# Optimization experiments

Hardware: AMD Instinct MI355X
Metric: run time of the kernel (lower is better)

The kernel has to match this reference:

```python
import jax, jax.numpy as jnp
import numpy as np

N, IN_FEAT, OUT_FEAT, H = 4096, 256, 256, 8
D = OUT_FEAT // H  # per-head dim = 32
ADJ_DENSITY = 0.05


def setup_inputs() -> dict:
    key = jax.random.key(0)
    kx, kw, kb, ka, kadj = jax.random.split(key, 5)
    x = jax.random.normal(kx, (N, IN_FEAT), dtype=jnp.float32)
    # eqx.nn.Linear params: weight [out, in], bias [out]
    W = jax.random.normal(kw, (OUT_FEAT, IN_FEAT), dtype=jnp.float32) * (1.0 / np.sqrt(IN_FEAT))
    b = jax.random.normal(kb, (OUT_FEAT,), dtype=jnp.float32) * 0.01
    a = jax.random.normal(ka, (H, 2 * D), dtype=jnp.float32)
    adj_matrix = jax.random.bernoulli(kadj, ADJ_DENSITY, (N, N)).astype(jnp.float32)
    return {"x": x, "W": W, "b": b, "a": a, "adj_matrix": adj_matrix}


def reference(x, W, b, a, adj_matrix):
    num_nodes = x.shape[0]
    num_heads = a.shape[0]
    half = a.shape[1] // 2
    # projection: [N, H*D] -> [N, H, D]
    node_feats = (x @ W.T + b).reshape(num_nodes, num_heads, half)
    # per-head additive attention halves -> [N, H]
    logit_parent = (node_feats * a[None, :, :half]).sum(axis=-1)
    logit_child = (node_feats * a[None, :, half:]).sum(axis=-1)
    # [N, N, H] dense logits via broadcast-add
    attn_logits = logit_parent[:, None, :] + logit_child[None, :, :]
    attn_logits = jax.nn.leaky_relu(attn_logits, 0.2)
    # NOTE: faithful to source — masked entries set to 0.0 (not -inf)
    attn_logits = jnp.where(jnp.abs(adj_matrix)[..., None] != 0.0, attn_logits, 0.0)
    attn_probs = jax.nn.softmax(attn_logits, axis=1)
    out = jnp.einsum('ijh,jhc->ihc', attn_probs, node_feats)
    return out.reshape(num_nodes, -1)
```

## Files before the change

### kernel.cpp

```cpp
#include <hip/hip_runtime.h>

#define NN    4096
#define OF    256
#define NH    8
#define MAXNZ 384

typedef __attribute__((ext_vector_type(8))) short short8;
typedef __attribute__((ext_vector_type(4))) float f32x4;

__device__ __forceinline__ float bf2f(unsigned int u) {
    union { unsigned int i; float f; } v; v.i = u << 16; return v.f;
}
__device__ __forceinline__ unsigned short f2bf(float f) {
    union { float f; unsigned int i; } v; v.f = f;
    unsigned int x = v.i;
    return (unsigned short)((x + 0x7fffu + ((x >> 16) & 1u)) >> 16);
}
__device__ __forceinline__ unsigned int pk2bf(float a, float b) {
    return (unsigned int)f2bf(a) | ((unsigned int)f2bf(b) << 16);
}

__global__ __launch_bounds__(256) void k_pre(
    const float* __restrict__ adjf, const float* __restrict__ Wf,
    int* __restrict__ flag, unsigned short* __restrict__ Wbh,
    unsigned short* __restrict__ Wbl, float* __restrict__ zbase)
{
    __shared__ int viol;
    int t = threadIdx.x;
    int gid = blockIdx.x * 256 + t;
    if (t == 0) viol = 0;
    __syncthreads();
    int bad = 0;
    for (int k = t; k < NN; k += 256) {
        float v = adjf[k];
        if (!(v == 0.0f || v == 1.0f)) bad = 1;
    }
    if (bad) atomicAdd(&viol, 1);
    __syncthreads();
    int f = viol > 0;
    if (t == 0) *flag = f;

    zbase[gid] = 0.f;
    if (gid < 256) zbase[65536 + gid] = 0.f;
    if (!f) {
        float v = Wf[gid];
        unsigned short h = f2bf(v);
        Wbh[gid] = h; Wbl[gid] = f2bf(v - bf2f(h));
    }
}

__global__ __launch_bounds__(256) void k_main(
    const void* __restrict__ xraw, const void* __restrict__ Wraw,
    const void* __restrict__ braw, const void* __restrict__ araw,
    const float* __restrict__ adjf, const int* __restrict__ flag,
    const unsigned short* __restrict__ Wbh, const unsigned short* __restrict__ Wbl,
    unsigned short* __restrict__ nfb, float* __restrict__ lp,
    float* __restrict__ lc, float* __restrict__ Stot,
    unsigned short* __restrict__ csr, int* __restrict__ nnz)
{
    __shared__ unsigned short xh[16][264], xl[16][264];
    __shared__ int wtot[4];

    int f = *flag;
    int t = threadIdx.x;
    int wave = t >> 6;
    int lane = t & 63;
    int bid = blockIdx.x;
    int bdiv3 = bid / 3;

    if (bid - bdiv3*3 == 0) {
        int tid  = bdiv3 * 4 + wave;
        int mt = tid >> 4, nt = tid & 15;
        int lr = lane & 15;
        int kq = (lane >> 4) * 8;

        if (!f) {
            const float* xsrc = (const float*)xraw + (size_t)mt * 4096;
            #pragma unroll
            for (int q = 0; q < 16; q++) {
                int e = t + 256*q;
                float v = xsrc[e];
                unsigned short h = f2bf(v);
                xh[e >> 8][e & 255] = h;
                xl[e >> 8][e & 255] = f2bf(v - bf2f(h));
            }
            __syncthreads();
        }

        size_t wo = (size_t)(nt*16 + lr)*OF + kq;
        f32x4 acc = {0.f, 0.f, 0.f, 0.f};
        if (f) {
            const short8* xp = reinterpret_cast<const short8*>(
                (const unsigned short*)xraw + (size_t)(mt*16 + lr)*OF + kq);
            const short8* wp = reinterpret_cast<const short8*>(
                (const unsigned short*)Wraw + wo);
            #pragma unroll
            for (int kk = 0; kk < OF/32; kk++)
                acc = __builtin_amdgcn_mfma_f32_16x16x32_bf16(xp[kk*4], wp[kk*4], acc, 0, 0, 0);
        } else {
            const short8* wh = reinterpret_cast<const short8*>(Wbh + wo);
            const short8* wl = reinterpret_cast<const short8*>(Wbl + wo);
            #pragma unroll
            for (int kk = 0; kk < OF/32; kk++) {
                short8 ah = *reinterpret_cast<const short8*>(&xh[lr][kk*32 + kq]);
                short8 al = *reinterpret_cast<const short8*>(&xl[lr][kk*32 + kq]);
                short8 bh = wh[kk*4], bl = wl[kk*4];
                acc = __builtin_amdgcn_mfma_f32_16x16x32_bf16(ah, bh, acc, 0, 0, 0);
                acc = __builtin_amdgcn_mfma_f32_16x16x32_bf16(ah, bl, acc, 0, 0, 0);
                acc = __builtin_amdgcn_mfma_f32_16x16x32_bf16(al, bh, acc, 0, 0, 0);
            }
        }

        int col  = nt*16 + lr;
        int row0 = mt*16 + (lane >> 4) * 4;
        int h = col >> 5, cc = col & 31;
        float bias, apar, achd;
        if (f) {
            bias = bf2f((unsigned int)((const unsigned short*)braw)[col]);
            apar = bf2f((unsigned int)((const unsigned short*)araw)[h*64 + cc]);
            achd = bf2f((unsigned int)((const unsigned short*)araw)[h*64 + 32 + cc]);
        } else {
            bias = ((const float*)braw)[col];
            apar = ((const float*)araw)[h*64 + cc];
            achd = ((const float*)araw)[h*64 + 32 + cc];
        }
        float st = 0.f, pr[4], cr[4];
        #pragma unroll
        for (int r = 0; r < 4; r++) {
            float v = acc[r] + bias;
            nfb[(size_t)(row0 + r) * OF + col] = f2bf(v);
            st += v;
            pr[r] = v * apar;
            cr[r] = v * achd;
        }
        #pragma unroll
        for (int m = 1; m <= 8; m <<= 1) {
            #pragma unroll
            for (int r = 0; r < 4; r++) {
                pr[r] += __shfl_xor(pr[r], m, 64);
                cr[r] += __shfl_xor(cr[r], m, 64);
            }
        }
        if ((lane & 15) == 0) {
            #pragma unroll
            for (int r = 0; r < 4; r++) {
                atomicAdd(&lp[(row0 + r) * NH + h], pr[r]);
                atomicAdd(&lc[(row0 + r) * NH + h], cr[r]);
            }
        }
        st += __shfl_down(st, 16, 64);
        st += __shfl_down(st, 32, 64);
        if (lane < 16) atomicAdd(&Stot[col], st);
    } else {
        int sid = bid - bdiv3 - 1;
        int r    = sid*2 + (wave >> 1);
        int half = wave & 1;

        unsigned int m32 = 0;
        if (f) {
            const uint4* ap = reinterpret_cast<const uint4*>(
                (const unsigned short*)adjf + (size_t)r * NN + half * 2048);
            #pragma unroll
            for (int g = 0; g < 4; g++) {
                uint4 v = ap[lane + 64*g];
                unsigned int wd[4] = {v.x, v.y, v.z, v.w};
                #pragma unroll
                for (int u = 0; u < 4; u++) {
                    if (wd[u] & 0xffffu) m32 |= 1u << (g*8 + 2*u);
                    if (wd[u] >> 16)     m32 |= 1u << (g*8 + 2*u + 1);
                }
            }
        } else {
            const uint4* ap = reinterpret_cast<const uint4*>(
                adjf + (size_t)r * NN + half * 2048);
            #pragma unroll
            for (int g = 0; g < 8; g++) {
                uint4 v = ap[lane + 64*g];
                if (v.x) m32 |= 1u << (g*4);
                if (v.y) m32 |= 1u << (g*4 + 1);
                if (v.z) m32 |= 1u << (g*4 + 2);
                if (v.w) m32 |= 1u << (g*4 + 3);
            }
        }

        int pc = __popc(m32);
        int pref = pc;
        #pragma unroll
        for (int off = 1; off < 64; off <<= 1) {
            int u = __shfl_up(pref, off, 64);
            if (lane >= off) pref += u;
        }
        if (lane == 63) wtot[wave] = pref;
        __syncthreads();
        int base = (wave == 1) ? wtot[0] : (wave == 3) ? wtot[2] : 0;
        if (lane == 0) {
            if (wave == 0) nnz[r] = min(wtot[0] + wtot[1], MAXNZ);
            if (wave == 2) nnz[r] = min(wtot[2] + wtot[3], MAXNZ);
        }
        int pos = base + pref - pc;
        unsigned int mm = m32;
        int jb = half * 2048;
        while (mm && pos < MAXNZ) {
            int q = __builtin_ctz(mm);
            mm &= mm - 1;
            int j = f ? (jb + lane*8 + ((q >> 3) << 9) + (q & 7))
                      : (jb + lane*4 + ((q >> 2) << 8) + (q & 3));
            csr[(size_t)r * MAXNZ + pos++] = (unsigned short)j;
        }
    }
}

__global__ __launch_bounds__(256, 8) void k_attn(
    const int* __restrict__ flag, const unsigned short* __restrict__ csr,
    const int* __restrict__ nnz,
    const float* __restrict__ lp, const float* __restrict__ lc,
    const unsigned short* __restrict__ nfb, const float* __restrict__ Stot,
    void* __restrict__ outv)
{
    __shared__ float lps[NH];
    __shared__ int   jro[MAXNZ];
    __shared__ float wlist[MAXNZ][NH];
    __shared__ float zred[256];
    __shared__ float gred[3][256];

    int i = blockIdx.x;
    int t = threadIdx.x;
    int lane = t & 63, wid = t >> 6;
    int f = *flag;
    if (t < NH) lps[t] = lp[i*NH + t];
    int n = min(nnz[i], MAXNZ);

    if (t < MAXNZ/8) {
        uint4 v = reinterpret_cast<const uint4*>(csr + (size_t)i * MAXNZ)[t];
        unsigned int ws[4] = {v.x, v.y, v.z, v.w};
        #pragma unroll
        for (int u = 0; u < 4; u++) {
            jro[t*8 + 2*u]     = (int)(ws[u] & 0xffffu) * OF;
            jro[t*8 + 2*u + 1] = (int)(ws[u] >> 16) * OF;
        }
    }
    __syncthreads();

    int h8 = t & 7, c32 = t >> 3;
    float lph = lps[h8];
    float zp = 0.f;
    int k3 = c32;
    for (; k3 + 32 < n; k3 += 64) {
        int j0 = jro[k3] >> 5, j1 = jro[k3 + 32] >> 5;
        float l0 = lc[j0 + h8], l1 = lc[j1 + h8];
        float s0 = lph + l0; s0 = s0 > 0.f ? s0 : 0.2f * s0;
        float s1 = lph + l1; s1 = s1 > 0.f ? s1 : 0.2f * s1;
        float w0 = __expf(fminf(s0, 70.f)) - 1.f;
        float w1 = __expf(fminf(s1, 70.f)) - 1.f;
        wlist[k3][h8] = w0; wlist[k3 + 32][h8] = w1;
        zp += w0 + w1;
    }
    if (k3 < n) {
        float s = lph + lc[(jro[k3] >> 5) + h8];
        s = s > 0.f ? s : 0.2f * s;
        float w = __expf(fminf(s, 70.f)) - 1.f;
        wlist[k3][h8] = w;
        zp += w;
    }
    zred[t] = zp;
    __syncthreads();

    int hh = lane >> 3;
    int c4 = lane * 4;
    float a0 = 0.f, a1 = 0.f, a2 = 0.f, a3 = 0.f;
    int k = wid;
    for (; k + 28 < n; k += 32) {
        int jj[8]; float ww[8];
        #pragma unroll
        for (int u = 0; u < 8; u++) {
            jj[u] = __builtin_amdgcn_readfirstlane(jro[k + 4*u]);
            ww[u] = wlist[k + 4*u][hh];
        }
        uint2 d[8];
        #pragma unroll
        for (int u = 0; u < 8; u++)
            d[u] = *reinterpret_cast<const uint2*>(nfb + jj[u] + c4);
        #pragma unroll
        for (int u = 0; u < 8; u++) {
            a0 += ww[u] * bf2f(d[u].x & 0xffffu);
            a1 += ww[u] * bf2f(d[u].x >> 16);
            a2 += ww[u] * bf2f(d[u].y & 0xffffu);
            a3 += ww[u] * bf2f(d[u].y >> 16);
        }
    }
    for (; k < n; k += 4) {
        int j = __builtin_amdgcn_readfirstlane(jro[k]);
        float w = wlist[k][hh];
        uint2 d = *reinterpret_cast<const uint2*>(nfb + j + c4);
        a0 += w * bf2f(d.x & 0xffffu);
        a1 += w * bf2f(d.x >> 16);
        a2 += w * bf2f(d.y & 0xffffu);
        a3 += w * bf2f(d.y >> 16);
    }
    if (wid) {
        gred[wid-1][c4]   = a0; gred[wid-1][c4+1] = a1;
        gred[wid-1][c4+2] = a2; gred[wid-1][c4+3] = a3;
    }
    __syncthreads();

    if (wid == 0) {
        float z = zred[lane] + zred[lane+64] + zred[lane+128] + zred[lane+192];
        z += __shfl_down(z, 32, 64);
        z += __shfl_down(z, 16, 64);
        z += __shfl_down(z, 8, 64);
        float zfull = __shfl(z, hh, 64);
        float iz = 1.0f / (4096.0f + zfull);
        a0 += gred[0][c4]   + gred[1][c4]   + gred[2][c4];
        a1 += gred[0][c4+1] + gred[1][c4+1] + gred[2][c4+1];
        a2 += gred[0][c4+2] + gred[1][c4+2] + gred[2][c4+2];
        a3 += gred[0][c4+3] + gred[1][c4+3] + gred[2][c4+3];
        float4 stv = *reinterpret_cast<const float4*>(Stot + c4);
        float o0 = (stv.x + a0) * iz;
        float o1 = (stv.y + a1) * iz;
        float o2 = (stv.z + a2) * iz;
        float o3 = (stv.w + a3) * iz;
        if (f) {
            uint2 pk; pk.x = pk2bf(o0, o1); pk.y = pk2bf(o2, o3);
            *reinterpret_cast<uint2*>((unsigned short*)outv + (size_t)i*OF + c4) = pk;
        } else {
            float4 o = {o0, o1, o2, o3};
            *reinterpret_cast<float4*>((float*)outv + (size_t)i*OF + c4) = o;
        }
    }
}

extern "C" void kernel_launch(void* const* d_in, const int* in_sizes, int n_in,
                              void* d_out, int out_size, void* d_ws, size_t ws_size,
                              hipStream_t stream) {
    const void* x   = d_in[0];
    const void* W   = d_in[1];
    const void* b   = d_in[2];
    const void* a   = d_in[3];
    const void* adj = d_in[4];

    char* ws = (char*)d_ws;
    const size_t MB = 1024u*1024u, KB = 1024u;
    unsigned short* nfb  = (unsigned short*)(ws);
    float*          lp   = (float*)(ws + 2*MB);
    float*          lc   = (float*)(ws + 2*MB + 128*KB);
    float*          Stot = (float*)(ws + 2*MB + 256*KB);
    int*            flag = (int*)(ws + 2*MB + 257*KB);
    unsigned short* csr  = (unsigned short*)(ws + 2*MB + 258*KB);
    int*            nnz  = (int*)(ws + 5*MB + 258*KB);
    unsigned short* Wbh  = (unsigned short*)(ws + 6*MB);
    unsigned short* Wbl  = (unsigned short*)(ws + 6*MB + 128*KB);

    k_pre  <<<256,  256, 0, stream>>>((const float*)adj, (const float*)W,
                                      flag, Wbh, Wbl, lp);
    k_main <<<3072, 256, 0, stream>>>(x, W, b, a, (const float*)adj, flag,
                                      Wbh, Wbl, nfb, lp, lc, Stot, csr, nnz);
    k_attn <<<NN,   256, 0, stream>>>(flag, csr, nnz, lp, lc, nfb, Stot, d_out);
}
```

Before: 155.0 us.

## Fold preprocessing kernel into main kernel and split W to bf16 hi/lo inline

```diff
diff --git a/kernel.cpp b/kernel.cpp
--- a/kernel.cpp
+++ b/kernel.cpp
@@ -20,53 +20,35 @@
     return (unsigned int)f2bf(a) | ((unsigned int)f2bf(b) << 16);
 }
 
-__global__ __launch_bounds__(256) void k_pre(
-    const float* __restrict__ adjf, const float* __restrict__ Wf,
-    int* __restrict__ flag, unsigned short* __restrict__ Wbh,
-    unsigned short* __restrict__ Wbl, float* __restrict__ zbase)
-{
-    __shared__ int viol;
-    int t = threadIdx.x;
-    int gid = blockIdx.x * 256 + t;
-    if (t == 0) viol = 0;
-    __syncthreads();
-    int bad = 0;
-    for (int k = t; k < NN; k += 256) {
-        float v = adjf[k];
-        if (!(v == 0.0f || v == 1.0f)) bad = 1;
-    }
-    if (bad) atomicAdd(&viol, 1);
-    __syncthreads();
-    int f = viol > 0;
-    if (t == 0) *flag = f;
-
-    zbase[gid] = 0.f;
-    if (gid < 256) zbase[65536 + gid] = 0.f;
-    if (!f) {
-        float v = Wf[gid];
-        unsigned short h = f2bf(v);
-        Wbh[gid] = h; Wbl[gid] = f2bf(v - bf2f(h));
-    }
-}
-
 __global__ __launch_bounds__(256) void k_main(
     const void* __restrict__ xraw, const void* __restrict__ Wraw,
     const void* __restrict__ braw, const void* __restrict__ araw,
-    const float* __restrict__ adjf, const int* __restrict__ flag,
-    const unsigned short* __restrict__ Wbh, const unsigned short* __restrict__ Wbl,
+    const float* __restrict__ adjf, int* __restrict__ flag,
     unsigned short* __restrict__ nfb, float* __restrict__ lp,
     float* __restrict__ lc, float* __restrict__ Stot,
     unsigned short* __restrict__ csr, int* __restrict__ nnz)
 {
     __shared__ unsigned short xh[16][264], xl[16][264];
     __shared__ int wtot[4];
-
-    int f = *flag;
+    __shared__ int viol;
+
     int t = threadIdx.x;
     int wave = t >> 6;
     int lane = t & 63;
     int bid = blockIdx.x;
     int bdiv3 = bid / 3;
+
+    if (t == 0) viol = 0;
+    __syncthreads();
+    int bad = 0;
+    for (int k = t; k < NN; k += 256) {
+        float v = adjf[k];
+        if (!(v == 0.0f || v == 1.0f)) bad = 1;
+    }
+    if (bad) atomicAdd(&viol, 1);
+    __syncthreads();
+    int f = viol > 0;
+    if (bid == 0 && t == 0) *flag = f;
 
     if (bid - bdiv3*3 == 0) {
         int tid  = bdiv3 * 4 + wave;
@@ -98,13 +80,20 @@
             for (int kk = 0; kk < OF/32; kk++)
                 acc = __builtin_amdgcn_mfma_f32_16x16x32_bf16(xp[kk*4], wp[kk*4], acc, 0, 0, 0);
         } else {
-            const short8* wh = reinterpret_cast<const short8*>(Wbh + wo);
-            const short8* wl = reinterpret_cast<const short8*>(Wbl + wo);
+            const float* wsrc = (const float*)Wraw + wo;
             #pragma unroll
             for (int kk = 0; kk < OF/32; kk++) {
                 short8 ah = *reinterpret_cast<const short8*>(&xh[lr][kk*32 + kq]);
                 short8 al = *reinterpret_cast<const short8*>(&xl[lr][kk*32 + kq]);
-                short8 bh = wh[kk*4], bl = wl[kk*4];
+                float4 w0 = *reinterpret_cast<const float4*>(wsrc + kk*32);
+                float4 w1 = *reinterpret_cast<const float4*>(wsrc + kk*32 + 4);
+                float wv[8] = {w0.x, w0.y, w0.z, w0.w, w1.x, w1.y, w1.z, w1.w};
+                short8 bh, bl;
+                #pragma unroll
+                for (int e = 0; e < 8; e++) {
+                    unsigned short h = f2bf(wv[e]);
+                    bh[e] = (short)h; bl[e] = (short)f2bf(wv[e] - bf2f(h));
+                }
                 acc = __builtin_amdgcn_mfma_f32_16x16x32_bf16(ah, bh, acc, 0, 0, 0);
                 acc = __builtin_amdgcn_mfma_f32_16x16x32_bf16(ah, bl, acc, 0, 0, 0);
                 acc = __builtin_amdgcn_mfma_f32_16x16x32_bf16(al, bh, acc, 0, 0, 0);
@@ -245,17 +234,24 @@
     float lph = lps[h8];
     float zp = 0.f;
     int k3 = c32;
-    for (; k3 + 32 < n; k3 += 64) {
-        int j0 = jro[k3] >> 5, j1 = jro[k3 + 32] >> 5;
+    for (; k3 + 96 < n; k3 += 128) {
+        int j0 = jro[k3] >> 5,      j1 = jro[k3 + 32] >> 5;
+        int j2 = jro[k3 + 64] >> 5, j3 = jro[k3 + 96] >> 5;
         float l0 = lc[j0 + h8], l1 = lc[j1 + h8];
+        float l2 = lc[j2 + h8], l3 = lc[j3 + h8];
         float s0 = lph + l0; s0 = s0 > 0.f ? s0 : 0.2f * s0;
         float s1 = lph + l1; s1 = s1 > 0.f ? s1 : 0.2f * s1;
+        float s2 = lph + l2; s2 = s2 > 0.f ? s2 : 0.2f * s2;
+        float s3 = lph + l3; s3 = s3 > 0.f ? s3 : 0.2f * s3;
         float w0 = __expf(fminf(s0, 70.f)) - 1.f;
         float w1 = __expf(fminf(s1, 70.f)) - 1.f;
-        wlist[k3][h8] = w0; wlist[k3 + 32][h8] = w1;
-        zp += w0 + w1;
-    }
-    if (k3 < n) {
+        float w2 = __expf(fminf(s2, 70.f)) - 1.f;
+        float w3 = __expf(fminf(s3, 70.f)) - 1.f;
+        wlist[k3][h8] = w0;      wlist[k3 + 32][h8] = w1;
+        wlist[k3 + 64][h8] = w2; wlist[k3 + 96][h8] = w3;
+        zp += (w0 + w1) + (w2 + w3);
+    }
+    for (; k3 < n; k3 += 32) {
         float s = lph + lc[(jro[k3] >> 5) + h8];
         s = s > 0.f ? s : 0.2f * s;
         float w = __expf(fminf(s, 70.f)) - 1.f;
@@ -347,12 +343,9 @@
     int*            flag = (int*)(ws + 2*MB + 257*KB);
     unsigned short* csr  = (unsigned short*)(ws + 2*MB + 258*KB);
     int*            nnz  = (int*)(ws + 5*MB + 258*KB);
-    unsigned short* Wbh  = (unsigned short*)(ws + 6*MB);
-    unsigned short* Wbl  = (unsigned short*)(ws + 6*MB + 128*KB);
-
-    k_pre  <<<256,  256, 0, stream>>>((const float*)adj, (const float*)W,
-                                      flag, Wbh, Wbl, lp);
+
+    hipMemsetAsync(lp, 0, 257*KB, stream);
     k_main <<<3072, 256, 0, stream>>>(x, W, b, a, (const float*)adj, flag,
-                                      Wbh, Wbl, nfb, lp, lc, Stot, csr, nnz);
+                                      nfb, lp, lc, Stot, csr, nnz);
     k_attn <<<NN,   256, 0, stream>>>(flag, csr, nnz, lp, lc, nfb, Stot, d_out);
 }
```

Measured after the change: 156.7 us. No clear change (+1.1%).
